# Performance work log

Measured on AMD Instinct MI355X. Metric: run time of the kernel, lower is better.

## Reference

```python
import jax, jax.numpy as jnp
import numpy as np

EPS = 1e-5

def _ln(x, g, b):
    mu = jnp.mean(x, axis=-1, keepdims=True)
    var = jnp.mean(jnp.square(x - mu), axis=-1, keepdims=True)
    return (x - mu) * jax.lax.rsqrt(var + EPS) * g + b

def setup_inputs() -> dict:
    key = jax.random.key(0)
    ks = jax.random.split(key, 12)
    B, N, CZ, CF, CP = 1, 512, 128, 384, 256
    s = 0.02
    return {
        'z': jax.random.normal(ks[0], (B, N, N, CZ), jnp.float32),
        'framepair_embed': jax.random.normal(ks[1], (B, N, N, CP), jnp.float32),
        'rigids_embed_flat': jax.random.normal(ks[2], (B, N, CF), jnp.float32),
        'rigids_to_res_idx': jax.random.randint(ks[3], (B, N), 0, N, dtype=jnp.int64),
        'rigids_mask': jnp.ones((B, N), jnp.float32),
        # nodepair_to_framepair_broadcast: LayerNorm(c_z) + Linear(c_z, c_framepair, bias=False)
        'ln_z_g': jnp.ones((CZ,), jnp.float32),
        'ln_z_b': jnp.zeros((CZ,), jnp.float32),
        'W_z': jax.random.normal(ks[4], (CZ, CP), jnp.float32) * s,
        # frame_ln + two bias-free broadcasts
        'ln_f_g': jnp.ones((CF,), jnp.float32),
        'ln_f_b': jnp.zeros((CF,), jnp.float32),
        'W_l': jax.random.normal(ks[5], (CF, CP), jnp.float32) * s,
        'W_m': jax.random.normal(ks[6], (CF, CP), jnp.float32) * s,
        # framepair_ffn: LN + Linear + ReLU + Linear + ReLU + Linear
        'ffn_ln_g': jnp.ones((CP,), jnp.float32),
        'ffn_ln_b': jnp.zeros((CP,), jnp.float32),
        'W1': jax.random.normal(ks[7], (CP, CP), jnp.float32) * s,
        'b1': jnp.zeros((CP,), jnp.float32),
        'W2': jax.random.normal(ks[8], (CP, CP), jnp.float32) * s,
        'b2': jnp.zeros((CP,), jnp.float32),
        'W3': jax.random.normal(ks[9], (CP, CP), jnp.float32) * s,
        'b3': jnp.zeros((CP,), jnp.float32),
    }

def reference(z, framepair_embed, rigids_embed_flat, rigids_to_res_idx, rigids_mask,
              ln_z_g, ln_z_b, W_z, ln_f_g, ln_f_b, W_l, W_m,
              ffn_ln_g, ffn_ln_b, W1, b1, W2, b2, W3, b3):
    # --- broadcast singles: row + column frame features into pair rep ---
    src = _ln(rigids_embed_flat, ln_f_g, ln_f_b)            # [B, N, CF]
    l = jnp.einsum('bnf,fp->bnp', src, W_l)                 # [B, N, CP]
    m = jnp.einsum('bnf,fp->bnp', src, W_m)
    fe = framepair_embed + l[:, :, None, :] + m[:, None, :, :]
    # --- broadcast pairs: irregular gather of residue-pair features ---
    ii = rigids_to_res_idx[0]                               # [N] (batch-0 indices, as in torch code)
    zb = z[:, ii[:, None], ii[None, :]]                     # [B, N, N, CZ]
    mk = rigids_mask[0]
    pair_mask = (mk[:, None] * mk[None, :])[None, :, :, None]
    zb = zb * pair_mask
    fe = fe + jnp.einsum('bijc,cp->bijp', _ln(zb, ln_z_g, ln_z_b), W_z)
    # --- framepair FFN with residual ---
    h = _ln(fe, ffn_ln_g, ffn_ln_b)
    h = jax.nn.relu(jnp.einsum('bijp,pq->bijq', h, W1) + b1)
    h = jax.nn.relu(jnp.einsum('bijp,pq->bijq', h, W2) + b2)
    fe = fe + jnp.einsum('bijp,pq->bijq', h, W3) + b3
    return fe
```

## Files before the change

### kernel.cpp

```cpp
#include <hip/hip_runtime.h>

#define NN 512
#define CZv 128
#define CFv 384
#define CPv 256

typedef __attribute__((ext_vector_type(8))) short s16x8;
typedef __attribute__((ext_vector_type(4))) short s16x4;
typedef __attribute__((ext_vector_type(4))) float f32x4;

__device__ __forceinline__ unsigned short f2bf(float f) {
  unsigned int u = __builtin_bit_cast(unsigned int, f);
  u = (u + 0x7FFFu + ((u >> 16) & 1u)) >> 16;
  return (unsigned short)u;
}

__global__ void pack_w(const float* __restrict__ W, short* __restrict__ Wf, int total) {
  int o = blockIdx.x * 256 + threadIdx.x;
  if (o >= total) return;
  int e = o & 7;
  int l = (o >> 3) & 63;
  int mt = (o >> 9) & 15;
  int kk = o >> 13;
  int k = kk * 32 + (l >> 4) * 8 + e;
  int p = mt * 16 + (l & 15);
  Wf[o] = (short)f2bf(W[k * 256 + p]);
}

__global__ __launch_bounds__(256) void lm_kernel(
    const float* __restrict__ rf, const float* __restrict__ g, const float* __restrict__ b,
    const float* __restrict__ Wl, const float* __restrict__ Wm,
    float* __restrict__ lout, float* __restrict__ mout) {
  __shared__ float S[8][CFv];
  const int tid = threadIdx.x;
  const int w = tid >> 6;
  const int lane = tid & 63;
  for (int rr = 0; rr < 2; ++rr) {
    int r = blockIdx.x * 8 + w * 2 + rr;
    const float* x = rf + (long)r * CFv;
    float v[6];
    float s1 = 0.f, s2 = 0.f;
#pragma unroll
    for (int q = 0; q < 6; ++q) {
      v[q] = x[lane + q * 64];
      s1 += v[q];
      s2 += v[q] * v[q];
    }
#pragma unroll
    for (int off = 1; off < 64; off <<= 1) {
      s1 += __shfl_xor(s1, off, 64);
      s2 += __shfl_xor(s2, off, 64);
    }
    float mu = s1 * (1.f / CFv);
    float va = s2 * (1.f / CFv) - mu * mu;
    float rs = rsqrtf(va + 1e-5f);
#pragma unroll
    for (int q = 0; q < 6; ++q) {
      int k = lane + q * 64;
      S[w * 2 + rr][k] = (v[q] - mu) * rs * g[k] + b[k];
    }
  }
  __syncthreads();
  float accl[8], accm[8];
#pragma unroll
  for (int r = 0; r < 8; ++r) { accl[r] = 0.f; accm[r] = 0.f; }
  for (int k = 0; k < CFv; ++k) {
    float wl = Wl[k * CPv + tid];
    float wm = Wm[k * CPv + tid];
#pragma unroll
    for (int r = 0; r < 8; ++r) {
      accl[r] += S[r][k] * wl;
      accm[r] += S[r][k] * wm;
    }
  }
#pragma unroll
  for (int r = 0; r < 8; ++r) {
    long rg = blockIdx.x * 8 + r;
    lout[rg * CPv + tid] = accl[r];
    mout[rg * CPv + tid] = accm[r];
  }
}

__global__ __launch_bounds__(256, 2) void fused_main(
    const float* __restrict__ z, const float* __restrict__ fpe,
    const int* __restrict__ idx, const float* __restrict__ msk,
    const float* __restrict__ lnzg, const float* __restrict__ lnzb,
    const float* __restrict__ ffng, const float* __restrict__ ffnb,
    const float* __restrict__ b1p, const float* __restrict__ b2p, const float* __restrict__ b3p,
    const float* __restrict__ lws, const float* __restrict__ mws,
    const short* __restrict__ Wzf, const short* __restrict__ W1f,
    const short* __restrict__ W2f, const short* __restrict__ W3f,
    float* __restrict__ out) {
  __shared__ __align__(16) char Xz[64 * CZv * 2];
  __shared__ __align__(16) char Xs[64 * CPv * 2];
  __shared__ float Ssum[4][64];
  __shared__ float Ssq[4][64];

  const int tid = threadIdx.x;
  const int w = tid >> 6;
  const int lane = tid & 63;
  const int l15 = lane & 15;
  const int lg = lane >> 4;

  const int tile = blockIdx.x;
  const int i = tile >> 3;
  const int j0 = (tile & 7) * 64;
  const int r0 = tile * 64;

  {
    const int row = w * 16 + l15;
    const int j = j0 + row;
    const int ia = idx[i];
    const int jb = idx[j];
    const float pm = msk[i] * msk[j];
    const float* zr = z + ((long)ia * NN + jb) * CZv;
    float zv[32];
    float s1 = 0.f, s2 = 0.f;
#pragma unroll
    for (int kk = 0; kk < 4; ++kk) {
      const f32x4* p = (const f32x4*)(zr + kk * 32 + lg * 8);
      f32x4 a = p[0];
      f32x4 c = p[1];
#pragma unroll
      for (int e = 0; e < 4; ++e) {
        zv[kk * 8 + e] = a[e] * pm;
        zv[kk * 8 + 4 + e] = c[e] * pm;
      }
    }
#pragma unroll
    for (int q = 0; q < 32; ++q) {
      s1 += zv[q];
      s2 += zv[q] * zv[q];
    }
    s1 += __shfl_xor(s1, 16, 64);
    s1 += __shfl_xor(s1, 32, 64);
    s2 += __shfl_xor(s2, 16, 64);
    s2 += __shfl_xor(s2, 32, 64);
    float mu = s1 * (1.f / CZv);
    float va = s2 * (1.f / CZv) - mu * mu;
    float rs = rsqrtf(va + 1e-5f);
    const int swz = (row & 7) << 4;
#pragma unroll
    for (int kk = 0; kk < 4; ++kk) {
      const f32x4* gp = (const f32x4*)(lnzg + kk * 32 + lg * 8);
      const f32x4* bp = (const f32x4*)(lnzb + kk * 32 + lg * 8);
      f32x4 g0 = gp[0], g1 = gp[1];
      f32x4 q0 = bp[0], q1 = bp[1];
      s16x8 hv;
#pragma unroll
      for (int e = 0; e < 4; ++e) {
        hv[e] = (short)f2bf((zv[kk * 8 + e] - mu) * rs * g0[e] + q0[e]);
        hv[4 + e] = (short)f2bf((zv[kk * 8 + 4 + e] - mu) * rs * g1[e] + q1[e]);
      }
      int off = (row * 256 + kk * 64 + lg * 16) ^ swz;
      *(s16x8*)(Xz + off) = hv;
    }
  }
  __syncthreads();

  f32x4 fe[4][4];
#pragma unroll
  for (int nt = 0; nt < 4; ++nt) {
    const int row = nt * 16 + l15;
    const long rg = (long)r0 + row;
    const float* fpr = fpe + rg * CPv;
    const float* lr = lws + (long)i * CPv;
    const float* mr = mws + (long)(j0 + row) * CPv;
#pragma unroll
    for (int mi = 0; mi < 4; ++mi) {
      const int c0 = (4 * w + mi) * 16 + lg * 4;
      f32x4 a = *(const f32x4*)(fpr + c0);
      f32x4 lb = *(const f32x4*)(lr + c0);
      f32x4 mb = *(const f32x4*)(mr + c0);
      fe[nt][mi] = a + lb + mb;
    }
  }

  {
    const s16x8* Wp = (const s16x8*)Wzf;
#pragma unroll
    for (int kk = 0; kk < 4; ++kk) {
      s16x8 bfr[4];
#pragma unroll
      for (int nt = 0; nt < 4; ++nt) {
        const int row = nt * 16 + l15;
        int off = (row * 256 + kk * 64 + lg * 16) ^ ((row & 7) << 4);
        bfr[nt] = *(const s16x8*)(Xz + off);
      }
#pragma unroll
      for (int mi = 0; mi < 4; ++mi) {
        s16x8 afr = Wp[(kk * 16 + 4 * w + mi) * 64 + lane];
#pragma unroll
        for (int nt = 0; nt < 4; ++nt)
          fe[nt][mi] = __builtin_amdgcn_mfma_f32_16x16x32_bf16(afr, bfr[nt], fe[nt][mi], 0, 0, 0);
      }
    }
  }

  float mu4[4], rs4[4];
  {
    float s[4], q[4];
#pragma unroll
    for (int nt = 0; nt < 4; ++nt) {
      s[nt] = 0.f;
      q[nt] = 0.f;
#pragma unroll
      for (int mi = 0; mi < 4; ++mi)
#pragma unroll
        for (int e = 0; e < 4; ++e) {
          float v = fe[nt][mi][e];
          s[nt] += v;
          q[nt] += v * v;
        }
      s[nt] += __shfl_xor(s[nt], 16, 64);
      s[nt] += __shfl_xor(s[nt], 32, 64);
      q[nt] += __shfl_xor(q[nt], 16, 64);
      q[nt] += __shfl_xor(q[nt], 32, 64);
    }
    if (lane < 16) {
#pragma unroll
      for (int nt = 0; nt < 4; ++nt) {
        Ssum[w][nt * 16 + lane] = s[nt];
        Ssq[w][nt * 16 + lane] = q[nt];
      }
    }
    __syncthreads();
#pragma unroll
    for (int nt = 0; nt < 4; ++nt) {
      const int row = nt * 16 + l15;
      float ts = Ssum[0][row] + Ssum[1][row] + Ssum[2][row] + Ssum[3][row];
      float tq = Ssq[0][row] + Ssq[1][row] + Ssq[2][row] + Ssq[3][row];
      float mu = ts * (1.f / CPv);
      float va = tq * (1.f / CPv) - mu * mu;
      mu4[nt] = mu;
      rs4[nt] = rsqrtf(va + 1e-5f);
    }
  }

  {
    f32x4 g4[4], b4[4];
#pragma unroll
    for (int mi = 0; mi < 4; ++mi) {
      const int c0 = (4 * w + mi) * 16 + lg * 4;
      g4[mi] = *(const f32x4*)(ffng + c0);
      b4[mi] = *(const f32x4*)(ffnb + c0);
    }
#pragma unroll
    for (int nt = 0; nt < 4; ++nt) {
      const int row = nt * 16 + l15;
      const int swz = (row & 7) << 4;
#pragma unroll
      for (int mi = 0; mi < 4; ++mi) {
        const int c0 = (4 * w + mi) * 16 + lg * 4;
        s16x4 hv;
#pragma unroll
        for (int e = 0; e < 4; ++e)
          hv[e] = (short)f2bf((fe[nt][mi][e] - mu4[nt]) * rs4[nt] * g4[mi][e] + b4[mi][e]);
        int off = (row * 512 + c0 * 2) ^ swz;
        *(s16x4*)(Xs + off) = hv;
      }
    }
  }
  __syncthreads();

  auto ffn_gemm = [&](const short* Wf, f32x4(&acc)[4][4]) {
    const s16x8* Wp = (const s16x8*)Wf;
#pragma unroll
    for (int kk = 0; kk < 8; ++kk) {
      s16x8 bfr[4];
#pragma unroll
      for (int nt = 0; nt < 4; ++nt) {
        const int row = nt * 16 + l15;
        int off = (row * 512 + kk * 64 + lg * 16) ^ ((row & 7) << 4);
        bfr[nt] = *(const s16x8*)(Xs + off);
      }
#pragma unroll
      for (int mi = 0; mi < 4; ++mi) {
        s16x8 afr = Wp[(kk * 16 + 4 * w + mi) * 64 + lane];
#pragma unroll
        for (int nt = 0; nt < 4; ++nt)
          acc[nt][mi] = __builtin_amdgcn_mfma_f32_16x16x32_bf16(afr, bfr[nt], acc[nt][mi], 0, 0, 0);
      }
    }
  };

  auto write_relu = [&](f32x4(&acc)[4][4]) {
#pragma unroll
    for (int nt = 0; nt < 4; ++nt) {
      const int row = nt * 16 + l15;
      const int swz = (row & 7) << 4;
#pragma unroll
      for (int mi = 0; mi < 4; ++mi) {
        const int c0 = (4 * w + mi) * 16 + lg * 4;
        s16x4 hv;
#pragma unroll
        for (int e = 0; e < 4; ++e) {
          float v = acc[nt][mi][e];
          v = v > 0.f ? v : 0.f;
          hv[e] = (short)f2bf(v);
        }
        int off = (row * 512 + c0 * 2) ^ swz;
        *(s16x4*)(Xs + off) = hv;
      }
    }
  };

  f32x4 hacc[4][4];
  {
    f32x4 bini[4];
#pragma unroll
    for (int mi = 0; mi < 4; ++mi)
      bini[mi] = *(const f32x4*)(b1p + (4 * w + mi) * 16 + lg * 4);
#pragma unroll
    for (int nt = 0; nt < 4; ++nt)
#pragma unroll
      for (int mi = 0; mi < 4; ++mi) hacc[nt][mi] = bini[mi];
  }
  ffn_gemm(W1f, hacc);
  __syncthreads();
  write_relu(hacc);
  __syncthreads();

  {
    f32x4 bini[4];
#pragma unroll
    for (int mi = 0; mi < 4; ++mi)
      bini[mi] = *(const f32x4*)(b2p + (4 * w + mi) * 16 + lg * 4);
#pragma unroll
    for (int nt = 0; nt < 4; ++nt)
#pragma unroll
      for (int mi = 0; mi < 4; ++mi) hacc[nt][mi] = bini[mi];
  }
  ffn_gemm(W2f, hacc);
  __syncthreads();
  write_relu(hacc);
  __syncthreads();

  ffn_gemm(W3f, fe);
  {
    f32x4 b34[4];
#pragma unroll
    for (int mi = 0; mi < 4; ++mi)
      b34[mi] = *(const f32x4*)(b3p + (4 * w + mi) * 16 + lg * 4);
#pragma unroll
    for (int nt = 0; nt < 4; ++nt) {
      const long rg = (long)r0 + nt * 16 + l15;
#pragma unroll
      for (int mi = 0; mi < 4; ++mi) {
        const int c0 = (4 * w + mi) * 16 + lg * 4;
        f32x4 o = fe[nt][mi] + b34[mi];
        *(f32x4*)(out + rg * CPv + c0) = o;
      }
    }
  }
}

extern "C" void kernel_launch(void* const* d_in, const int* in_sizes, int n_in,
                              void* d_out, int out_size, void* d_ws, size_t ws_size,
                              hipStream_t stream) {
  const float* z = (const float*)d_in[0];
  const float* fpe = (const float*)d_in[1];
  const float* rf = (const float*)d_in[2];
  const int* idx = (const int*)d_in[3];
  const float* msk = (const float*)d_in[4];
  const float* lnzg = (const float*)d_in[5];
  const float* lnzb = (const float*)d_in[6];
  const float* Wz = (const float*)d_in[7];
  const float* lnfg = (const float*)d_in[8];
  const float* lnfb = (const float*)d_in[9];
  const float* Wl = (const float*)d_in[10];
  const float* Wm = (const float*)d_in[11];
  const float* ffng = (const float*)d_in[12];
  const float* ffnb = (const float*)d_in[13];
  const float* W1 = (const float*)d_in[14];
  const float* b1 = (const float*)d_in[15];
  const float* W2 = (const float*)d_in[16];
  const float* b2 = (const float*)d_in[17];
  const float* W3 = (const float*)d_in[18];
  const float* b3 = (const float*)d_in[19];
  float* out = (float*)d_out;

  char* ws = (char*)d_ws;
  float* lws = (float*)ws;
  float* mws = (float*)(ws + 512 * 1024);
  short* Wzf = (short*)(ws + 1024 * 1024);
  short* W1f = (short*)(ws + 1024 * 1024 + 64 * 1024);
  short* W2f = (short*)(ws + 1024 * 1024 + 192 * 1024);
  short* W3f = (short*)(ws + 1024 * 1024 + 320 * 1024);

  pack_w<<<128, 256, 0, stream>>>(Wz, Wzf, 128 * 256);
  pack_w<<<256, 256, 0, stream>>>(W1, W1f, 256 * 256);
  pack_w<<<256, 256, 0, stream>>>(W2, W2f, 256 * 256);
  pack_w<<<256, 256, 0, stream>>>(W3, W3f, 256 * 256);
  lm_kernel<<<64, 256, 0, stream>>>(rf, lnfg, lnfb, Wl, Wm, lws, mws);
  fused_main<<<4096, 256, 0, stream>>>(z, fpe, idx, msk, lnzg, lnzb, ffng, ffnb,
                                       b1, b2, b3, lws, mws, Wzf, W1f, W2f, W3f, out);
}
```

Measured before the change: 353.2 us.

## Cut LDS and register footprint to raise occupancy in fused pair kernel

Merges the two LDS staging buffers into one shared buffer. It keeps the residual fe in bf16 (packed 4-short vectors) across the FFN instead of fp32, so the accumulator registers can be reused for the final GEMM. It also hoists the fe/l/m loads before the z gather, loads the row-l vector once, and raises launch bounds to 4 blocks per CU. The intent is more waves per CU to hide memory latency. The cost is a precision loss on the residual path, since fe is rounded to bf16 before the W3 output is added.

```diff
diff --git a/kernel.cpp b/kernel.cpp
--- a/kernel.cpp
+++ b/kernel.cpp
@@ -13,6 +13,10 @@
   unsigned int u = __builtin_bit_cast(unsigned int, f);
   u = (u + 0x7FFFu + ((u >> 16) & 1u)) >> 16;
   return (unsigned short)u;
+}
+__device__ __forceinline__ float bf2f(unsigned short h) {
+  unsigned int u = ((unsigned int)h) << 16;
+  return __builtin_bit_cast(float, u);
 }
 
 __global__ void pack_w(const float* __restrict__ W, short* __restrict__ Wf, int total) {
@@ -81,7 +85,7 @@
   }
 }
 
-__global__ __launch_bounds__(256, 2) void fused_main(
+__global__ __launch_bounds__(256, 4) void fused_main(
     const float* __restrict__ z, const float* __restrict__ fpe,
     const int* __restrict__ idx, const float* __restrict__ msk,
     const float* __restrict__ lnzg, const float* __restrict__ lnzb,
@@ -91,8 +95,7 @@
     const short* __restrict__ Wzf, const short* __restrict__ W1f,
     const short* __restrict__ W2f, const short* __restrict__ W3f,
     float* __restrict__ out) {
-  __shared__ __align__(16) char Xz[64 * CZv * 2];
-  __shared__ __align__(16) char Xs[64 * CPv * 2];
+  __shared__ __align__(16) char X[64 * CPv * 2];
   __shared__ float Ssum[4][64];
   __shared__ float Ssq[4][64];
 
@@ -106,6 +109,29 @@
   const int i = tile >> 3;
   const int j0 = (tile & 7) * 64;
   const int r0 = tile * 64;
+
+  f32x4 fe[4][4];
+  {
+    f32x4 lb[4];
+    const float* lr = lws + (long)i * CPv;
+#pragma unroll
+    for (int mi = 0; mi < 4; ++mi)
+      lb[mi] = *(const f32x4*)(lr + (4 * w + mi) * 16 + lg * 4);
+#pragma unroll
+    for (int nt = 0; nt < 4; ++nt) {
+      const int row = nt * 16 + l15;
+      const long rg = (long)r0 + row;
+      const float* fpr = fpe + rg * CPv;
+      const float* mr = mws + (long)(j0 + row) * CPv;
+#pragma unroll
+      for (int mi = 0; mi < 4; ++mi) {
+        const int c0 = (4 * w + mi) * 16 + lg * 4;
+        f32x4 a = *(const f32x4*)(fpr + c0);
+        f32x4 mb = *(const f32x4*)(mr + c0);
+        fe[nt][mi] = a + lb[mi] + mb;
+      }
+    }
+  }
 
   {
     const int row = w * 16 + l15;
@@ -153,28 +179,10 @@
         hv[4 + e] = (short)f2bf((zv[kk * 8 + 4 + e] - mu) * rs * g1[e] + q1[e]);
       }
       int off = (row * 256 + kk * 64 + lg * 16) ^ swz;
-      *(s16x8*)(Xz + off) = hv;
-    }
-  }
-  __syncthreads();
-
-  f32x4 fe[4][4];
-#pragma unroll
-  for (int nt = 0; nt < 4; ++nt) {
-    const int row = nt * 16 + l15;
-    const long rg = (long)r0 + row;
-    const float* fpr = fpe + rg * CPv;
-    const float* lr = lws + (long)i * CPv;
-    const float* mr = mws + (long)(j0 + row) * CPv;
-#pragma unroll
-    for (int mi = 0; mi < 4; ++mi) {
-      const int c0 = (4 * w + mi) * 16 + lg * 4;
-      f32x4 a = *(const f32x4*)(fpr + c0);
-      f32x4 lb = *(const f32x4*)(lr + c0);
-      f32x4 mb = *(const f32x4*)(mr + c0);
-      fe[nt][mi] = a + lb + mb;
-    }
-  }
+      *(s16x8*)(X + off) = hv;
+    }
+  }
+  __syncthreads();
 
   {
     const s16x8* Wp = (const s16x8*)Wzf;
@@ -185,7 +193,7 @@
       for (int nt = 0; nt < 4; ++nt) {
         const int row = nt * 16 + l15;
         int off = (row * 256 + kk * 64 + lg * 16) ^ ((row & 7) << 4);
-        bfr[nt] = *(const s16x8*)(Xz + off);
+        bfr[nt] = *(const s16x8*)(X + off);
       }
 #pragma unroll
       for (int mi = 0; mi < 4; ++mi) {
@@ -237,6 +245,7 @@
     }
   }
 
+  s16x4 fe16[4][4];
   {
     f32x4 g4[4], b4[4];
 #pragma unroll
@@ -252,12 +261,16 @@
 #pragma unroll
       for (int mi = 0; mi < 4; ++mi) {
         const int c0 = (4 * w + mi) * 16 + lg * 4;
-        s16x4 hv;
-#pragma unroll
-        for (int e = 0; e < 4; ++e)
-          hv[e] = (short)f2bf((fe[nt][mi][e] - mu4[nt]) * rs4[nt] * g4[mi][e] + b4[mi][e]);
+        s16x4 hv, fv;
+#pragma unroll
+        for (int e = 0; e < 4; ++e) {
+          float v = fe[nt][mi][e];
+          hv[e] = (short)f2bf((v - mu4[nt]) * rs4[nt] * g4[mi][e] + b4[mi][e]);
+          fv[e] = (short)f2bf(v);
+        }
+        fe16[nt][mi] = fv;
         int off = (row * 512 + c0 * 2) ^ swz;
-        *(s16x4*)(Xs + off) = hv;
+        *(s16x4*)(X + off) = hv;
       }
     }
   }
@@ -272,7 +285,7 @@
       for (int nt = 0; nt < 4; ++nt) {
         const int row = nt * 16 + l15;
         int off = (row * 512 + kk * 64 + lg * 16) ^ ((row & 7) << 4);
-        bfr[nt] = *(const s16x8*)(Xs + off);
+        bfr[nt] = *(const s16x8*)(X + off);
       }
 #pragma unroll
       for (int mi = 0; mi < 4; ++mi) {
@@ -300,7 +313,7 @@
           hv[e] = (short)f2bf(v);
         }
         int off = (row * 512 + c0 * 2) ^ swz;
-        *(s16x4*)(Xs + off) = hv;
+        *(s16x4*)(X + off) = hv;
       }
     }
   };
@@ -336,21 +349,27 @@
   write_relu(hacc);
   __syncthreads();
 
-  ffn_gemm(W3f, fe);
   {
     f32x4 b34[4];
 #pragma unroll
     for (int mi = 0; mi < 4; ++mi)
       b34[mi] = *(const f32x4*)(b3p + (4 * w + mi) * 16 + lg * 4);
 #pragma unroll
-    for (int nt = 0; nt < 4; ++nt) {
-      const long rg = (long)r0 + nt * 16 + l15;
-#pragma unroll
-      for (int mi = 0; mi < 4; ++mi) {
-        const int c0 = (4 * w + mi) * 16 + lg * 4;
-        f32x4 o = fe[nt][mi] + b34[mi];
-        *(f32x4*)(out + rg * CPv + c0) = o;
-      }
+    for (int nt = 0; nt < 4; ++nt)
+#pragma unroll
+      for (int mi = 0; mi < 4; ++mi)
+#pragma unroll
+        for (int e = 0; e < 4; ++e)
+          hacc[nt][mi][e] = bf2f((unsigned short)fe16[nt][mi][e]) + b34[mi][e];
+  }
+  ffn_gemm(W3f, hacc);
+#pragma unroll
+  for (int nt = 0; nt < 4; ++nt) {
+    const long rg = (long)r0 + nt * 16 + l15;
+#pragma unroll
+    for (int mi = 0; mi < 4; ++mi) {
+      const int c0 = (4 * w + mi) * 16 + lg * 4;
+      *(f32x4*)(out + rg * CPv + c0) = hacc[nt][mi];
     }
   }
 }
```

New measurement: 668.8 us. +89.4%, slower.
